# Performance work log

Measured on AMD Instinct MI355X. Metric: run time of the kernel, lower is better.

## Reference

```python
import jax, jax.numpy as jnp
import numpy as np

N_NODES = 100_000
N_EDGES = 1_600_000
F_IN = 32
F_OUT = 32


def setup_inputs() -> dict:
    key = jax.random.key(0)
    kx, kr, kc, kv, kw = jax.random.split(key, 5)
    x = jax.random.normal(kx, (N_NODES, F_IN), dtype=jnp.float32)
    # COO adjacency: rows sorted (CSR-like locality), cols random, positive norm weights
    rows = jnp.sort(jax.random.randint(kr, (N_EDGES,), 0, N_NODES, dtype=jnp.int64))
    cols = jax.random.randint(kc, (N_EDGES,), 0, N_NODES, dtype=jnp.int64)
    vals = jax.random.uniform(kv, (N_EDGES,), dtype=jnp.float32)
    weight = jax.random.normal(kw, (F_IN, F_OUT), dtype=jnp.float32) / np.sqrt(F_IN)
    return {"x": x, "rows": rows, "cols": cols, "vals": vals, "weight": weight}


def reference(x, rows, cols, vals, weight):
    # z = A_hat @ x  (COO SpMM, equivalent to the distributed gather+spmm+allreduce)
    gathered = x[cols] * vals[:, None]                       # [E, F_in] edge messages
    z = jax.ops.segment_sum(gathered, rows, num_segments=x.shape[0])  # [N, F_in]
    # feature transform: z @ W (done in GCNFunc after broad_func)
    return z @ weight                                        # [N, F_out]
```

## Files before the change

kernel.cpp:

```cpp
#include <hip/hip_runtime.h>

#define F 32

typedef float v4f __attribute__((ext_vector_type(4)));

__device__ __forceinline__ unsigned int f2bf_rne(float f) {
    unsigned int u = __float_as_uint(f);
    return (u + 0x7fffu + ((u >> 16) & 1u)) >> 16;
}
__device__ __forceinline__ float bf_lo(unsigned int u) { return __uint_as_float(u << 16); }
__device__ __forceinline__ float bf_hi(unsigned int u) { return __uint_as_float(u & 0xffff0000u); }

__device__ __forceinline__ unsigned int enc_edge(int c, float v) {
    unsigned int q = (unsigned int)(v * 32768.0f + 0.5f);
    if (q > 32767u) q = 32767u;
    return (unsigned int)c | (q << 17);
}

__global__ void prep_kernel(const float* __restrict__ x, const float* __restrict__ w,
                            uint4* __restrict__ y4,
                            const int* __restrict__ rows,
                            const int* __restrict__ cols, const float* __restrict__ vals,
                            unsigned int* __restrict__ pk,
                            int* __restrict__ row_ptr,
                            int n_nodes, int n_edges, int gxw) {
    int b = blockIdx.x;
    if (b < gxw) {
        int n = b * blockDim.x + threadIdx.x;
        if (n >= n_nodes) return;
        const float4* xp = (const float4*)(x + (size_t)n * F);
        float xr[F];
#pragma unroll
        for (int j = 0; j < 8; ++j) {
            float4 t = xp[j];
            xr[4*j+0] = t.x; xr[4*j+1] = t.y; xr[4*j+2] = t.z; xr[4*j+3] = t.w;
        }
        float acc[F];
#pragma unroll
        for (int f = 0; f < F; ++f) acc[f] = 0.f;
#pragma unroll
        for (int k = 0; k < F; ++k) {
            float xk = xr[k];
#pragma unroll
            for (int f = 0; f < F; ++f)
                acc[f] = fmaf(xk, w[k * F + f], acc[f]);
        }
        unsigned int op[16];
#pragma unroll
        for (int k = 0; k < 16; ++k)
            op[k] = f2bf_rne(acc[2*k]) | (f2bf_rne(acc[2*k+1]) << 16);
#pragma unroll
        for (int j = 0; j < 4; ++j)
            y4[(size_t)n * 4 + j] = make_uint4(op[4*j], op[4*j+1], op[4*j+2], op[4*j+3]);
    } else {
        int e = (b - gxw) * blockDim.x + threadIdx.x;
        if (e > n_edges) return;
        if (e < n_edges)
            __builtin_nontemporal_store(enc_edge(cols[e], vals[e]), &pk[e]);
        int prev = (e == 0) ? -1 : rows[e - 1];
        int cur  = (e == n_edges) ? n_nodes : rows[e];
        for (int r = prev + 1; r <= cur; ++r) row_ptr[r] = e;
    }
}

__global__ void spmm_kernel(const uint4* __restrict__ y4,
                            const unsigned int* __restrict__ pk,
                            const int* __restrict__ row_ptr,
                            v4f* __restrict__ out4, int n_nodes) {
    int gid = blockIdx.x * blockDim.x + threadIdx.x;
    int n = gid >> 2;
    int l = gid & 3;
    if (n >= n_nodes) return;

    int e0 = row_ptr[n];
    int e1 = row_ptr[n + 1];
    float a0 = 0.f, a1 = 0.f, a2 = 0.f, a3 = 0.f,
          a4 = 0.f, a5 = 0.f, a6 = 0.f, a7 = 0.f;

    for (int base = e0; base < e1; base += 8) {
        unsigned int p[8];
#pragma unroll
        for (int j = 0; j < 8; ++j) {
            int idx = base + j;
            p[j] = __builtin_nontemporal_load(&pk[idx < e1 ? idx : e0]);
        }
        int   c[8]; float v[8];
#pragma unroll
        for (int j = 0; j < 8; ++j) {
            c[j] = (int)(p[j] & 0x1ffffu);
            v[j] = (base + j < e1) ? (float)(p[j] >> 17) * (1.0f / 32768.0f) : 0.f;
        }
        uint4 u[8];
#pragma unroll
        for (int j = 0; j < 8; ++j)
            u[j] = y4[(size_t)c[j] * 4 + l];
#pragma unroll
        for (int j = 0; j < 8; ++j) {
            a0 += bf_lo(u[j].x) * v[j];  a1 += bf_hi(u[j].x) * v[j];
            a2 += bf_lo(u[j].y) * v[j];  a3 += bf_hi(u[j].y) * v[j];
            a4 += bf_lo(u[j].z) * v[j];  a5 += bf_hi(u[j].z) * v[j];
            a6 += bf_lo(u[j].w) * v[j];  a7 += bf_hi(u[j].w) * v[j];
        }
    }
    v4f* op = out4 + (size_t)n * 8 + l * 2;
    v4f o0; o0[0] = a0; o0[1] = a1; o0[2] = a2; o0[3] = a3;
    v4f o1; o1[0] = a4; o1[1] = a5; o1[2] = a6; o1[3] = a7;
    __builtin_nontemporal_store(o0, &op[0]);
    __builtin_nontemporal_store(o1, &op[1]);
}

extern "C" void kernel_launch(void* const* d_in, const int* in_sizes, int n_in,
                              void* d_out, int out_size, void* d_ws, size_t ws_size,
                              hipStream_t stream) {
    const float* x    = (const float*)d_in[0];
    const int*   rows = (const int*)d_in[1];
    const int*   cols = (const int*)d_in[2];
    const float* vals = (const float*)d_in[3];
    const float* w    = (const float*)d_in[4];

    int n_nodes = in_sizes[0] / F;
    int n_edges = in_sizes[1];

    uint4*        y4      = (uint4*)d_ws;
    unsigned int* pk      = (unsigned int*)(y4 + (size_t)n_nodes * 4);
    int*          row_ptr = (int*)(pk + (size_t)n_edges);

    int gxw = (n_nodes + 255) / 256;
    int gpe = (n_edges + 1 + 255) / 256;
    prep_kernel<<<gxw + gpe, 256, 0, stream>>>(x, w, y4, rows, cols, vals,
                                               pk, row_ptr, n_nodes, n_edges, gxw);

    int grid_spmm = (n_nodes * 4 + 255) / 256;
    spmm_kernel<<<grid_spmm, 256, 0, stream>>>(y4, pk, row_ptr,
                                               (v4f*)d_out, n_nodes);
}
```

Before: 58.04 us.

## Drop packed edge array; use 16 lanes per row with shuffled edge indices

Removes the prep-stage packing of cols/vals into a quantized 32-bit word. The SpMM now reads cols and vals directly, with 16 lanes per row instead of 4. Each lane loads one edge's col/val cooperatively and broadcasts it via shuffles, then gathers one 32-bit bf16 pair per edge. This avoids writing and re-reading the packed array and the lossy value quantization, but reads 8 bytes per edge instead of 4 and issues narrower gathers with more threads per row.

```diff
diff --git a/kernel.cpp b/kernel.cpp
--- a/kernel.cpp
+++ b/kernel.cpp
@@ -2,7 +2,7 @@
 
 #define F 32
 
-typedef float v4f __attribute__((ext_vector_type(4)));
+typedef float v2f __attribute__((ext_vector_type(2)));
 
 __device__ __forceinline__ unsigned int f2bf_rne(float f) {
     unsigned int u = __float_as_uint(f);
@@ -11,17 +11,9 @@
 __device__ __forceinline__ float bf_lo(unsigned int u) { return __uint_as_float(u << 16); }
 __device__ __forceinline__ float bf_hi(unsigned int u) { return __uint_as_float(u & 0xffff0000u); }
 
-__device__ __forceinline__ unsigned int enc_edge(int c, float v) {
-    unsigned int q = (unsigned int)(v * 32768.0f + 0.5f);
-    if (q > 32767u) q = 32767u;
-    return (unsigned int)c | (q << 17);
-}
-
 __global__ void prep_kernel(const float* __restrict__ x, const float* __restrict__ w,
                             uint4* __restrict__ y4,
                             const int* __restrict__ rows,
-                            const int* __restrict__ cols, const float* __restrict__ vals,
-                            unsigned int* __restrict__ pk,
                             int* __restrict__ row_ptr,
                             int n_nodes, int n_edges, int gxw) {
     int b = blockIdx.x;
@@ -55,58 +47,48 @@
     } else {
         int e = (b - gxw) * blockDim.x + threadIdx.x;
         if (e > n_edges) return;
-        if (e < n_edges)
-            __builtin_nontemporal_store(enc_edge(cols[e], vals[e]), &pk[e]);
         int prev = (e == 0) ? -1 : rows[e - 1];
         int cur  = (e == n_edges) ? n_nodes : rows[e];
         for (int r = prev + 1; r <= cur; ++r) row_ptr[r] = e;
     }
 }
 
-__global__ void spmm_kernel(const uint4* __restrict__ y4,
-                            const unsigned int* __restrict__ pk,
+__global__ void spmm_kernel(const unsigned int* __restrict__ y_u,
+                            const int* __restrict__ cols,
+                            const float* __restrict__ vals,
                             const int* __restrict__ row_ptr,
-                            v4f* __restrict__ out4, int n_nodes) {
+                            v2f* __restrict__ out2, int n_nodes) {
     int gid = blockIdx.x * blockDim.x + threadIdx.x;
-    int n = gid >> 2;
-    int l = gid & 3;
+    int n = gid >> 4;
+    int l = gid & 15;
     if (n >= n_nodes) return;
 
     int e0 = row_ptr[n];
     int e1 = row_ptr[n + 1];
-    float a0 = 0.f, a1 = 0.f, a2 = 0.f, a3 = 0.f,
-          a4 = 0.f, a5 = 0.f, a6 = 0.f, a7 = 0.f;
+    float aL = 0.f, aH = 0.f;
 
-    for (int base = e0; base < e1; base += 8) {
-        unsigned int p[8];
+    for (int base = e0; base < e1; base += 16) {
+        int idx  = base + l;
+        bool ok  = idx < e1;
+        int idxc = ok ? idx : (e1 - 1);
+        int   cB = __builtin_nontemporal_load(&cols[idxc]);
+        float vB = ok ? __builtin_nontemporal_load(&vals[idxc]) : 0.f;
+
+        unsigned int u[16];
 #pragma unroll
-        for (int j = 0; j < 8; ++j) {
-            int idx = base + j;
-            p[j] = __builtin_nontemporal_load(&pk[idx < e1 ? idx : e0]);
+        for (int j = 0; j < 16; ++j) {
+            int c = __shfl(cB, j, 16);
+            u[j] = y_u[(size_t)c * 16 + l];
         }
-        int   c[8]; float v[8];
 #pragma unroll
-        for (int j = 0; j < 8; ++j) {
-            c[j] = (int)(p[j] & 0x1ffffu);
-            v[j] = (base + j < e1) ? (float)(p[j] >> 17) * (1.0f / 32768.0f) : 0.f;
-        }
-        uint4 u[8];
-#pragma unroll
-        for (int j = 0; j < 8; ++j)
-            u[j] = y4[(size_t)c[j] * 4 + l];
-#pragma unroll
-        for (int j = 0; j < 8; ++j) {
-            a0 += bf_lo(u[j].x) * v[j];  a1 += bf_hi(u[j].x) * v[j];
-            a2 += bf_lo(u[j].y) * v[j];  a3 += bf_hi(u[j].y) * v[j];
-            a4 += bf_lo(u[j].z) * v[j];  a5 += bf_hi(u[j].z) * v[j];
-            a6 += bf_lo(u[j].w) * v[j];  a7 += bf_hi(u[j].w) * v[j];
+        for (int j = 0; j < 16; ++j) {
+            float v = __shfl(vB, j, 16);
+            aL += bf_lo(u[j]) * v;
+            aH += bf_hi(u[j]) * v;
         }
     }
-    v4f* op = out4 + (size_t)n * 8 + l * 2;
-    v4f o0; o0[0] = a0; o0[1] = a1; o0[2] = a2; o0[3] = a3;
-    v4f o1; o1[0] = a4; o1[1] = a5; o1[2] = a6; o1[3] = a7;
-    __builtin_nontemporal_store(o0, &op[0]);
-    __builtin_nontemporal_store(o1, &op[1]);
+    v2f o; o[0] = aL; o[1] = aH;
+    __builtin_nontemporal_store(o, &out2[(size_t)n * 16 + l]);
 }
 
 extern "C" void kernel_launch(void* const* d_in, const int* in_sizes, int n_in,
@@ -121,16 +103,15 @@
     int n_nodes = in_sizes[0] / F;
     int n_edges = in_sizes[1];
 
-    uint4*        y4      = (uint4*)d_ws;
-    unsigned int* pk      = (unsigned int*)(y4 + (size_t)n_nodes * 4);
-    int*          row_ptr = (int*)(pk + (size_t)n_edges);
+    uint4* y4      = (uint4*)d_ws;
+    int*   row_ptr = (int*)((char*)d_ws + (size_t)n_nodes * 16 * sizeof(unsigned int));
 
     int gxw = (n_nodes + 255) / 256;
     int gpe = (n_edges + 1 + 255) / 256;
-    prep_kernel<<<gxw + gpe, 256, 0, stream>>>(x, w, y4, rows, cols, vals,
-                                               pk, row_ptr, n_nodes, n_edges, gxw);
+    prep_kernel<<<gxw + gpe, 256, 0, stream>>>(x, w, y4, rows, row_ptr,
+                                               n_nodes, n_edges, gxw);
 
-    int grid_spmm = (n_nodes * 4 + 255) / 256;
-    spmm_kernel<<<grid_spmm, 256, 0, stream>>>(y4, pk, row_ptr,
-                                               (v4f*)d_out, n_nodes);
+    int grid_spmm = (n_nodes * 16 + 255) / 256;
+    spmm_kernel<<<grid_spmm, 256, 0, stream>>>((const unsigned int*)y4, cols, vals,
+                                               row_ptr, (v2f*)d_out, n_nodes);
 }
```

Result: faster. 51.16 us (-11.9%).
